# Optimization experiments

Measured on AMD Instinct MI355X. Metric: run time of the kernel, lower is better.

Reference implementation:

```python
import jax, jax.numpy as jnp
import numpy as np

B, T, E, H = 4, 2048, 1024, 16
D = E // H  # head_size = 64

def setup_inputs() -> dict:
    key = jax.random.key(0)
    ks = jax.random.split(key, 8)
    s = 1.0 / np.sqrt(E)
    inp = {
        'k': jax.random.normal(ks[0], (B, T, E), jnp.float32),
        'q': jax.random.normal(ks[1], (B, T, E), jnp.float32),
        'v': jax.random.normal(ks[2], (B, T, E), jnp.float32),
        'mask': jnp.triu(jnp.ones((T, T), jnp.bool_), k=1),  # True above diagonal -> masked
        # per-head projection weights stacked: [H, E, D], no bias (bias=False)
        'Wk': jax.random.uniform(ks[3], (H, E, D), jnp.float32, -s, s),
        'Wq': jax.random.uniform(ks[4], (H, E, D), jnp.float32, -s, s),
        'Wv': jax.random.uniform(ks[5], (H, E, D), jnp.float32, -s, s),
        # output projection (bias=True default)
        'Wp': jax.random.uniform(ks[6], (E, E), jnp.float32, -s, s),
        'bp': jax.random.uniform(ks[7], (E,), jnp.float32, -s, s),
    }
    return inp

def reference(k, q, v, mask, Wk, Wq, Wv, Wp, bp):
    # per-head projections (bias=False Linears), batched over heads
    xk = jnp.einsum('bte,hed->bhtd', k, Wk)
    xq = jnp.einsum('bte,hed->bhtd', q, Wq)
    xv = jnp.einsum('bte,hed->bhtd', v, Wv)
    # NOTE: original scales by sqrt(C) where C = embed_size (input dim), not head_size
    wei = jnp.einsum('bhtd,bhsd->bhts', xq, xk) / jnp.sqrt(jnp.asarray(E, xq.dtype))
    wei = jnp.where(mask, -jnp.inf, wei)  # masked_fill(mask, -inf)
    wei = jax.nn.softmax(wei, axis=-1)
    out = jnp.einsum('bhts,bhsd->bhtd', wei, xv)
    out = out.transpose(0, 2, 1, 3).reshape(B, T, E)  # concat heads on last dim
    return out @ Wp.T + bp
```

## Files before the change

kernel.cpp:

```cpp
#include <hip/hip_runtime.h>
#include <cstdint>
#include <cstddef>


#define B_ 4
#define T_ 2048
#define E_ 1024
#define H_ 16
#define D_ 64
#define MROWS 8192
#define MK    8388608
#define SCALE_LOG2E 0.045084220027780106f

typedef unsigned short u16;
typedef unsigned int   u32;
typedef __attribute__((ext_vector_type(4))) float  f32x4;
typedef __attribute__((ext_vector_type(4))) u32    u32x4;
typedef __attribute__((ext_vector_type(8))) u16    u16x8;
typedef __attribute__((ext_vector_type(8))) __bf16 bf16x8;

typedef __attribute__((address_space(1))) void gvoid_t;
typedef __attribute__((address_space(3))) void lvoid_t;

__device__ __forceinline__ void async_load16(const void* g, void* l) {
  __builtin_amdgcn_global_load_lds((gvoid_t*)(uintptr_t)g, (lvoid_t*)l, 16, 0, 0);
}

__device__ __forceinline__ u16 f2bf(float f) {
  u32 u = __builtin_bit_cast(u32, f);
  u = (u + 0x7FFFu + ((u >> 16) & 1u)) >> 16;
  return (u16)u;
}

__device__ __forceinline__ u16 f2bf_hw(float f) {
  return __builtin_bit_cast(u16, (__bf16)f);
}

__device__ __forceinline__ float fast_exp2(float x) {
#if __has_builtin(__builtin_amdgcn_exp2f)
  return __builtin_amdgcn_exp2f(x);
#else
  return exp2f(x);
#endif
}

__device__ __forceinline__ bf16x8 ldfrag(const u16* p) {
  u32x4 t = *(const u32x4*)p;
  return __builtin_bit_cast(bf16x8, t);
}

__device__ __forceinline__ bf16x8 ldfrag_g(const u16* p) {
  u32x4 t = *(const u32x4*)p;
  return __builtin_bit_cast(bf16x8, t);
}

__device__ __forceinline__ f32x4 mfma_bf16(bf16x8 a, bf16x8 b, f32x4 c) {
  return __builtin_amdgcn_mfma_f32_16x16x32_bf16(a, b, c, 0, 0, 0);
}

__global__ __launch_bounds__(256) void cast_qkv_kernel(
    const float* __restrict__ q, const float* __restrict__ k,
    const float* __restrict__ v, u16* __restrict__ dst) {
  const int z = blockIdx.y;
  const float* src = (z == 0) ? q : (z == 1) ? k : v;
  const float sc = (z == 0) ? SCALE_LOG2E : 1.0f;
  u16* out = dst + (size_t)z * MK;
  size_t i0 = ((size_t)blockIdx.x * 256 + threadIdx.x) * 8;
  float4 a = *(const float4*)(src + i0);
  float4 b = *(const float4*)(src + i0 + 4);
  u16x8 o;
  o[0] = f2bf_hw(a.x * sc); o[1] = f2bf_hw(a.y * sc);
  o[2] = f2bf_hw(a.z * sc); o[3] = f2bf_hw(a.w * sc);
  o[4] = f2bf_hw(b.x * sc); o[5] = f2bf_hw(b.y * sc);
  o[6] = f2bf_hw(b.z * sc); o[7] = f2bf_hw(b.w * sc);
  *(u16x8*)(out + i0) = o;
}

__global__ __launch_bounds__(256) void prep_weights_kernel(
    const float* __restrict__ Wq, const float* __restrict__ Wk,
    const float* __restrict__ Wv, const float* __restrict__ Wp,
    u16* __restrict__ dstW, u16* __restrict__ dstWp) {
  const int z = blockIdx.y;
  const int t = blockIdx.x * 256 + threadIdx.x;
  if (z == 3) { dstWp[t] = f2bf(Wp[t]); return; }
  const float* W = (z == 0) ? Wq : (z == 1) ? Wk : Wv;
  const int j = t >> 10, e = t & 1023;
  const int h = j >> 6, d = j & 63;
  dstW[(size_t)z * (E_ * E_) + t] = f2bf(W[h * (E_ * D_) + e * D_ + d]);
}

template <int FINAL>
__global__ __launch_bounds__(256) void gemm_bt_kernel(
    const u16* __restrict__ Abase, const u16* __restrict__ Btbase,
    u16* __restrict__ Cb, float* __restrict__ Cf,
    const float* __restrict__ bias) {
  constexpr int Md = 8192, Nd = 1024, Kd = 1024;
  __shared__ __align__(16) u16 As[128 * 32];
  __shared__ __align__(16) u16 Bs[128 * 32];
  const int tid = threadIdx.x;
  const int wave = tid >> 6, lane = tid & 63;
  const int l16 = lane & 15, quad = lane >> 4;
  const int z = blockIdx.z;
  const u16* A  = Abase  + (size_t)z * Md * Kd;
  const u16* Bt = Btbase + (size_t)z * Nd * Kd;
  const int tm = blockIdx.x * 128, tn = blockIdx.y * 128;
  const int wm = (wave >> 1) * 64, wn = (wave & 1) * 64;

  f32x4 acc[4][4];
#pragma unroll
  for (int i = 0; i < 4; ++i)
#pragma unroll
    for (int j = 0; j < 4; ++j) acc[i][j] = f32x4{0.f, 0.f, 0.f, 0.f};

  const int row0 = tid >> 2, seg = tid & 3;
  const u16* Ag0 = A  + (size_t)(tm + row0) * Kd + seg * 8;
  const u16* Ag1 = Ag0 + (size_t)64 * Kd;
  const u16* Bg0 = Bt + (size_t)(tn + row0) * Kd + seg * 8;
  const u16* Bg1 = Bg0 + (size_t)64 * Kd;
  char* AsB = (char*)&As[0];
  char* BsB = (char*)&Bs[0];
  const int wbase = wave * 1024;

  for (int kt = 0; kt < Kd / 32; ++kt) {
    async_load16(Ag0, AsB + wbase);
    async_load16(Ag1, AsB + 4096 + wbase);
    async_load16(Bg0, BsB + wbase);
    async_load16(Bg1, BsB + 4096 + wbase);
    Ag0 += 32; Ag1 += 32; Bg0 += 32; Bg1 += 32;
    __syncthreads();
    bf16x8 af[4], bfr[4];
#pragma unroll
    for (int i = 0; i < 4; ++i) {
      af[i]  = ldfrag(&As[(wm + i * 16 + l16) * 32 + quad * 8]);
      bfr[i] = ldfrag(&Bs[(wn + i * 16 + l16) * 32 + quad * 8]);
    }
#pragma unroll
    for (int mi = 0; mi < 4; ++mi)
#pragma unroll
      for (int ni = 0; ni < 4; ++ni)
        acc[mi][ni] = mfma_bf16(af[mi], bfr[ni], acc[mi][ni]);
    __syncthreads();
  }

  if (FINAL) {
    float bv[4];
#pragma unroll
    for (int ni = 0; ni < 4; ++ni) bv[ni] = bias[tn + wn + ni * 16 + l16];
#pragma unroll
    for (int mi = 0; mi < 4; ++mi)
#pragma unroll
      for (int r = 0; r < 4; ++r) {
        const int row = tm + wm + mi * 16 + quad * 4 + r;
        float* cp = Cf + (size_t)row * Nd + tn + wn;
#pragma unroll
        for (int ni = 0; ni < 4; ++ni)
          cp[ni * 16 + l16] = acc[mi][ni][r] + bv[ni];
      }
  } else {
    u16* C = Cb + (size_t)z * Md * Nd;
#pragma unroll
    for (int mi = 0; mi < 4; ++mi)
#pragma unroll
      for (int r = 0; r < 4; ++r) {
        const int row = tm + wm + mi * 16 + quad * 4 + r;
        u16* cp = C + (size_t)row * Nd + tn + wn;
#pragma unroll
        for (int ni = 0; ni < 4; ++ni)
          cp[ni * 16 + l16] = f2bf(acc[mi][ni][r]);
      }
  }
}

__global__ __launch_bounds__(256, 3) void attn_kernel(
    const u16* __restrict__ Xq, const u16* __restrict__ Xk,
    const u16* __restrict__ Xv, u16* __restrict__ Xo) {
  const int qt = 15 - blockIdx.y;
  const int bh = blockIdx.x;
  const int b = bh >> 4, h = bh & 15;
  const int tid = threadIdx.x, wave = tid >> 6, lane = tid & 63;
  const int l16 = lane & 15, quad = lane >> 4;

  __shared__ __align__(16) u16 Ks[2 * 4096];
  __shared__ __align__(16) u16 Vts[2 * 4608];
  __shared__ __align__(16) u16 Ps[128 * 72];

  const size_t base = (size_t)b * T_ * E_ + h * 64;
  const u16* Qp = Xq + base + (size_t)qt * 128 * E_;
  const u16* Kp = Xk + base;
  const u16* Vp = Xv + base;
  char* KsB = (char*)&Ks[0];

  const int kk8 = lane & 3;

  auto stageK = [&](int kt, int buf) {
#pragma unroll
    for (int i = 0; i < 2; ++i) {
      const int c = wave + i * 4;
      const int ks = c >> 2, rb = (c & 3) * 16;
      const int row = rb + (lane >> 2);
      async_load16(Kp + (size_t)(kt * 64 + row) * E_ + ks * 32 + kk8 * 8,
                   KsB + buf * 8192 + ks * 4096 + rb * 64);
    }
  };
  auto loadV = [&](int kt, u32x4* vreg) {
#pragma unroll
    for (int i = 0; i < 2; ++i) {
      const int dseg = wave + i * 4;
      vreg[i] = *(const u32x4*)(Vp + (size_t)(kt * 64 + lane) * E_ + dseg * 8);
    }
  };
  auto writeV = [&](int buf, const u32x4* vreg) {
#pragma unroll
    for (int i = 0; i < 2; ++i) {
      const int dseg = wave + i * 4;
      union { u32x4 v; u16 s[8]; } t; t.v = vreg[i];
#pragma unroll
      for (int ii = 0; ii < 8; ++ii)
        Vts[buf * 4608 + (dseg * 8 + ii) * 72 + lane] = t.s[ii];
    }
  };

  bf16x8 qf[2][2];
#pragma unroll
  for (int mi = 0; mi < 2; ++mi)
#pragma unroll
    for (int ks = 0; ks < 2; ++ks)
      qf[mi][ks] = ldfrag_g(Qp + (size_t)(wave * 32 + mi * 16 + l16) * E_ +
                            ks * 32 + quad * 8);

  u16x8 ones_u;
#pragma unroll
  for (int i = 0; i < 8; ++i) ones_u[i] = 0x3F80;
  const bf16x8 ones = __builtin_bit_cast(bf16x8, ones_u);

  f32x4 o_acc[2][4];
#pragma unroll
  for (int mi = 0; mi < 2; ++mi)
#pragma unroll
    for (int di = 0; di < 4; ++di) o_acc[mi][di] = f32x4{0.f, 0.f, 0.f, 0.f};
  f32x4 lrow[2] = {f32x4{0.f, 0.f, 0.f, 0.f}, f32x4{0.f, 0.f, 0.f, 0.f}};

  {
    u32x4 vreg[2];
    stageK(0, 0);
    loadV(0, vreg);
    writeV(0, vreg);
  }

  const int kt_end = 2 * qt + 1;
  for (int kt = 0; kt <= kt_end; ++kt) {
    const int buf = kt & 1;
    __syncthreads();

    bf16x8 kf[4][2];
#pragma unroll
    for (int ni = 0; ni < 4; ++ni)
#pragma unroll
      for (int ks = 0; ks < 2; ++ks)
        kf[ni][ks] = ldfrag(&Ks[buf * 4096 + ks * 2048 + (ni * 16 + l16) * 32 +
                                quad * 8]);

    f32x4 sa[2][4];
#pragma unroll
    for (int mi = 0; mi < 2; ++mi)
#pragma unroll
      for (int ni = 0; ni < 4; ++ni) {
        f32x4 s = f32x4{0.f, 0.f, 0.f, 0.f};
        s = mfma_bf16(qf[mi][0], kf[ni][0], s);
        s = mfma_bf16(qf[mi][1], kf[ni][1], s);
        sa[mi][ni] = s;
      }

    u32x4 vreg[2];
    const bool have_next = (kt < kt_end);
    if (have_next) {
      stageK(kt + 1, buf ^ 1);
      loadV(kt + 1, vreg);
    }

    if (kt >= 2 * qt) {
#pragma unroll
      for (int mi = 0; mi < 2; ++mi) {
        const int grow0 = qt * 128 + wave * 32 + mi * 16 + quad * 4;
#pragma unroll
        for (int ni = 0; ni < 4; ++ni) {
          const int gcol = kt * 64 + ni * 16 + l16;
#pragma unroll
          for (int r = 0; r < 4; ++r)
            if (gcol > grow0 + r) sa[mi][ni][r] = -INFINITY;
        }
      }
    }

#pragma unroll
    for (int mi = 0; mi < 2; ++mi) {
#pragma unroll
      for (int ni = 0; ni < 4; ++ni)
#pragma unroll
        for (int r = 0; r < 4; ++r)
          sa[mi][ni][r] = fast_exp2(sa[mi][ni][r]);
#pragma unroll
      for (int ni = 0; ni < 4; ++ni)
#pragma unroll
        for (int r = 0; r < 4; ++r)
          Ps[(wave * 32 + mi * 16 + quad * 4 + r) * 72 + ni * 16 + l16] =
              f2bf_hw(sa[mi][ni][r]);
    }

    if (have_next) writeV(buf ^ 1, vreg);

    bf16x8 pf[2][2], vf[4][2];
#pragma unroll
    for (int mi = 0; mi < 2; ++mi)
#pragma unroll
      for (int ks = 0; ks < 2; ++ks)
        pf[mi][ks] = ldfrag(&Ps[(wave * 32 + mi * 16 + l16) * 72 + ks * 32 +
                                quad * 8]);
#pragma unroll
    for (int di = 0; di < 4; ++di)
#pragma unroll
      for (int ks = 0; ks < 2; ++ks)
        vf[di][ks] = ldfrag(&Vts[buf * 4608 + (di * 16 + l16) * 72 + ks * 32 +
                                 quad * 8]);
#pragma unroll
    for (int mi = 0; mi < 2; ++mi) {
      lrow[mi] = mfma_bf16(pf[mi][0], ones, lrow[mi]);
      lrow[mi] = mfma_bf16(pf[mi][1], ones, lrow[mi]);
#pragma unroll
      for (int di = 0; di < 4; ++di) {
        o_acc[mi][di] = mfma_bf16(pf[mi][0], vf[di][0], o_acc[mi][di]);
        o_acc[mi][di] = mfma_bf16(pf[mi][1], vf[di][1], o_acc[mi][di]);
      }
    }
  }

  u16* Op = Xo + base + (size_t)qt * 128 * E_;
#pragma unroll
  for (int mi = 0; mi < 2; ++mi)
#pragma unroll
    for (int r = 0; r < 4; ++r) {
      const float inv = 1.0f / lrow[mi][r];
      const int row = wave * 32 + mi * 16 + quad * 4 + r;
#pragma unroll
      for (int di = 0; di < 4; ++di)
        Op[(size_t)row * E_ + di * 16 + l16] = f2bf_hw(o_acc[mi][di][r] * inv);
    }
}

extern "C" void kernel_launch(void* const* d_in, const int* in_sizes, int n_in,
                              void* d_out, int out_size, void* d_ws, size_t ws_size,
                              hipStream_t stream) {
  const float* k_in = (const float*)d_in[0];
  const float* q_in = (const float*)d_in[1];
  const float* v_in = (const float*)d_in[2];
  const float* Wk = (const float*)d_in[4];
  const float* Wq = (const float*)d_in[5];
  const float* Wv = (const float*)d_in[6];
  const float* Wp = (const float*)d_in[7];
  const float* bp = (const float*)d_in[8];
  float* out = (float*)d_out;

  char* ws = (char*)d_ws;
  u16* qkvb = (u16*)ws;
  u16* Wt   = (u16*)(ws + 50331648);
  u16* Wpb  = (u16*)(ws + 56623104);
  u16* X    = (u16*)(ws + 58720256);
  u16* Xo   = (u16*)ws;

  cast_qkv_kernel<<<dim3(4096, 3), 256, 0, stream>>>(q_in, k_in, v_in, qkvb);
  prep_weights_kernel<<<dim3(4096, 4), 256, 0, stream>>>(Wq, Wk, Wv, Wp, Wt, Wpb);
  gemm_bt_kernel<0><<<dim3(64, 8, 3), 256, 0, stream>>>(qkvb, Wt, X, nullptr, nullptr);
  attn_kernel<<<dim3(64, 16), 256, 0, stream>>>(X, X + (size_t)MK, X + (size_t)2 * MK, Xo);
  gemm_bt_kernel<1><<<dim3(64, 8, 1), 256, 0, stream>>>(Xo, Wpb, nullptr, out, bp);
}
```

Measured before the change: 326.9 us.

## Replace GEMM with 256x256 double-buffered pipelined kernel using swizzled LDS

Replaces the 128x128, single-buffered, K=32 GEMM with a 256x256-tile, 512-thread kernel. It stages K=64 slices into double-buffered LDS with an XOR swizzle and interleaves async global loads with the MFMA phases. Explicit vmcnt waits, sched barriers and setprio control the overlap. This targets barrier stalls, global-load latency and LDS bank conflicts in the projection GEMMs. The cost is more registers and LDS per block, and fewer blocks in flight.

```diff
diff --git a/kernel.cpp b/kernel.cpp
--- a/kernel.cpp
+++ b/kernel.cpp
@@ -90,64 +90,164 @@
 }
 
 template <int FINAL>
-__global__ __launch_bounds__(256) void gemm_bt_kernel(
+__global__ __launch_bounds__(512, 2) void gemm256_kernel(
     const u16* __restrict__ Abase, const u16* __restrict__ Btbase,
     u16* __restrict__ Cb, float* __restrict__ Cf,
     const float* __restrict__ bias) {
   constexpr int Md = 8192, Nd = 1024, Kd = 1024;
-  __shared__ __align__(16) u16 As[128 * 32];
-  __shared__ __align__(16) u16 Bs[128 * 32];
+  constexpr int NT = Kd / 64;
+  constexpr int NJ = NT / 2;
+  __shared__ __align__(16) u16 AS[2][16384];
+  __shared__ __align__(16) u16 BS[2][16384];
   const int tid = threadIdx.x;
   const int wave = tid >> 6, lane = tid & 63;
   const int l16 = lane & 15, quad = lane >> 4;
+  const int wm = (wave >> 2) * 128;
+  const int wn = (wave & 3) * 64;
   const int z = blockIdx.z;
   const u16* A  = Abase  + (size_t)z * Md * Kd;
   const u16* Bt = Btbase + (size_t)z * Nd * Kd;
-  const int tm = blockIdx.x * 128, tn = blockIdx.y * 128;
-  const int wm = (wave >> 1) * 64, wn = (wave & 1) * 64;
-
-  f32x4 acc[4][4];
-#pragma unroll
-  for (int i = 0; i < 4; ++i)
-#pragma unroll
-    for (int j = 0; j < 4; ++j) acc[i][j] = f32x4{0.f, 0.f, 0.f, 0.f};
-
-  const int row0 = tid >> 2, seg = tid & 3;
-  const u16* Ag0 = A  + (size_t)(tm + row0) * Kd + seg * 8;
-  const u16* Ag1 = Ag0 + (size_t)64 * Kd;
-  const u16* Bg0 = Bt + (size_t)(tn + row0) * Kd + seg * 8;
-  const u16* Bg1 = Bg0 + (size_t)64 * Kd;
-  char* AsB = (char*)&As[0];
-  char* BsB = (char*)&Bs[0];
-  const int wbase = wave * 1024;
-
-  for (int kt = 0; kt < Kd / 32; ++kt) {
-    async_load16(Ag0, AsB + wbase);
-    async_load16(Ag1, AsB + 4096 + wbase);
-    async_load16(Bg0, BsB + wbase);
-    async_load16(Bg1, BsB + 4096 + wbase);
-    Ag0 += 32; Ag1 += 32; Bg0 += 32; Bg1 += 32;
-    __syncthreads();
-    bf16x8 af[4], bfr[4];
-#pragma unroll
-    for (int i = 0; i < 4; ++i) {
-      af[i]  = ldfrag(&As[(wm + i * 16 + l16) * 32 + quad * 8]);
-      bfr[i] = ldfrag(&Bs[(wn + i * 16 + l16) * 32 + quad * 8]);
-    }
+  const int tm = blockIdx.x * 256, tn = blockIdx.y * 256;
+
+  f32x4 acc[8][4];
+#pragma unroll
+  for (int i = 0; i < 8; ++i)
+#pragma unroll
+    for (int jj = 0; jj < 4; ++jj) acc[i][jj] = f32x4{0.f, 0.f, 0.f, 0.f};
+
+  char* ASB = (char*)&AS[0][0];
+  char* BSB = (char*)&BS[0][0];
+  const int r8  = lane >> 3;
+  const int csw = (lane & 7) ^ r8;
+  const int srow = wave * 8 + r8;
+
+  auto stA = [&](int t, int q) {
+    if (t < NT)
+      async_load16(A + (size_t)(tm + q * 64 + srow) * Kd + t * 64 + csw * 8,
+                   ASB + (t & 1) * 32768 + q * 8192 + wave * 1024);
+  };
+  auto stB = [&](int t, int q) {
+    if (t < NT)
+      async_load16(Bt + (size_t)(tn + q * 64 + srow) * Kd + t * 64 + csw * 8,
+                   BSB + (t & 1) * 32768 + q * 8192 + wave * 1024);
+  };
+  auto ldA = [&](int buf, int mi, int ks) -> bf16x8 {
+    const int row = wm + mi * 16 + l16;
+    const int ch  = (ks * 4 + quad) ^ (l16 & 7);
+    return ldfrag(&AS[buf][row * 64 + ch * 8]);
+  };
+  auto ldB = [&](int buf, int ni, int ks) -> bf16x8 {
+    const int row = wn + ni * 16 + l16;
+    const int ch  = (ks * 4 + quad) ^ (l16 & 7);
+    return ldfrag(&BS[buf][row * 64 + ch * 8]);
+  };
+
+  bf16x8 af[4][2], bf[4][2];
+
+#define GBAR() __builtin_amdgcn_s_barrier()
+#define PHASE_END()                       \
+  __builtin_amdgcn_sched_barrier(0);      \
+  GBAR()
+#define MFMA_QUAD(MB, NB)                                                   \
+  __builtin_amdgcn_s_setprio(1);                                            \
+  _Pragma("unroll") for (int mi = 0; mi < 4; ++mi)                          \
+  _Pragma("unroll") for (int ni = 0; ni < 2; ++ni)                          \
+  _Pragma("unroll") for (int ks = 0; ks < 2; ++ks)                          \
+      acc[(MB) + mi][(NB) + ni] = mfma_bf16(                                \
+          af[mi][ks], bf[(NB) + ni][ks], acc[(MB) + mi][(NB) + ni]);        \
+  __builtin_amdgcn_s_setprio(0)
+
+  stA(0, 0); stA(0, 2); stB(0, 0); stB(0, 1);
+  stA(0, 1); stA(0, 3); stB(0, 2); stB(0, 3);
+  stA(1, 0); stA(1, 2); stB(1, 0); stB(1, 1); stA(1, 1); stA(1, 3);
+  asm volatile("s_waitcnt vmcnt(6)" ::: "memory");
+  GBAR();
+
+  for (int j = 0; j < NJ; ++j) {
+    const int u = 2 * j;
 #pragma unroll
     for (int mi = 0; mi < 4; ++mi)
 #pragma unroll
-      for (int ni = 0; ni < 4; ++ni)
-        acc[mi][ni] = mfma_bf16(af[mi], bfr[ni], acc[mi][ni]);
-    __syncthreads();
+      for (int ks = 0; ks < 2; ++ks) af[mi][ks] = ldA(0, mi, ks);
+#pragma unroll
+    for (int ni = 0; ni < 2; ++ni)
+#pragma unroll
+      for (int ks = 0; ks < 2; ++ks) bf[ni][ks] = ldB(0, ni, ks);
+    stB(u + 1, 2); stB(u + 1, 3);
+    GBAR();
+    MFMA_QUAD(0, 0);
+    PHASE_END();
+#pragma unroll
+    for (int ni = 2; ni < 4; ++ni)
+#pragma unroll
+      for (int ks = 0; ks < 2; ++ks) bf[ni][ks] = ldB(0, ni, ks);
+    stA(u + 2, 0); stA(u + 2, 2);
+    GBAR();
+    MFMA_QUAD(0, 2);
+    PHASE_END();
+#pragma unroll
+    for (int mi = 0; mi < 4; ++mi)
+#pragma unroll
+      for (int ks = 0; ks < 2; ++ks) af[mi][ks] = ldA(0, mi + 4, ks);
+    stB(u + 2, 0); stB(u + 2, 1);
+    GBAR();
+    MFMA_QUAD(4, 0);
+    PHASE_END();
+    stA(u + 2, 1); stA(u + 2, 3);
+    GBAR();
+    MFMA_QUAD(4, 2);
+    __builtin_amdgcn_sched_barrier(0);
+    if (j == NJ - 1) {
+      asm volatile("s_waitcnt vmcnt(0)" ::: "memory");
+    } else {
+      asm volatile("s_waitcnt vmcnt(6)" ::: "memory");
+    }
+    GBAR();
+#pragma unroll
+    for (int mi = 0; mi < 4; ++mi)
+#pragma unroll
+      for (int ks = 0; ks < 2; ++ks) af[mi][ks] = ldA(1, mi, ks);
+#pragma unroll
+    for (int ni = 0; ni < 2; ++ni)
+#pragma unroll
+      for (int ks = 0; ks < 2; ++ks) bf[ni][ks] = ldB(1, ni, ks);
+    stB(u + 2, 2); stB(u + 2, 3);
+    GBAR();
+    MFMA_QUAD(0, 0);
+    PHASE_END();
+#pragma unroll
+    for (int ni = 2; ni < 4; ++ni)
+#pragma unroll
+      for (int ks = 0; ks < 2; ++ks) bf[ni][ks] = ldB(1, ni, ks);
+    stA(u + 3, 0); stA(u + 3, 2);
+    GBAR();
+    MFMA_QUAD(0, 2);
+    PHASE_END();
+#pragma unroll
+    for (int mi = 0; mi < 4; ++mi)
+#pragma unroll
+      for (int ks = 0; ks < 2; ++ks) af[mi][ks] = ldA(1, mi + 4, ks);
+    stB(u + 3, 0); stB(u + 3, 1);
+    GBAR();
+    MFMA_QUAD(4, 0);
+    PHASE_END();
+    stA(u + 3, 1); stA(u + 3, 3);
+    GBAR();
+    MFMA_QUAD(4, 2);
+    __builtin_amdgcn_sched_barrier(0);
+    asm volatile("s_waitcnt vmcnt(6)" ::: "memory");
+    GBAR();
   }
+#undef MFMA_QUAD
+#undef PHASE_END
+#undef GBAR
 
   if (FINAL) {
     float bv[4];
 #pragma unroll
     for (int ni = 0; ni < 4; ++ni) bv[ni] = bias[tn + wn + ni * 16 + l16];
 #pragma unroll
-    for (int mi = 0; mi < 4; ++mi)
+    for (int mi = 0; mi < 8; ++mi)
 #pragma unroll
       for (int r = 0; r < 4; ++r) {
         const int row = tm + wm + mi * 16 + quad * 4 + r;
@@ -159,7 +259,7 @@
   } else {
     u16* C = Cb + (size_t)z * Md * Nd;
 #pragma unroll
-    for (int mi = 0; mi < 4; ++mi)
+    for (int mi = 0; mi < 8; ++mi)
 #pragma unroll
       for (int r = 0; r < 4; ++r) {
         const int row = tm + wm + mi * 16 + quad * 4 + r;
@@ -369,7 +469,7 @@
 
   cast_qkv_kernel<<<dim3(4096, 3), 256, 0, stream>>>(q_in, k_in, v_in, qkvb);
   prep_weights_kernel<<<dim3(4096, 4), 256, 0, stream>>>(Wq, Wk, Wv, Wp, Wt, Wpb);
-  gemm_bt_kernel<0><<<dim3(64, 8, 3), 256, 0, stream>>>(qkvb, Wt, X, nullptr, nullptr);
+  gemm256_kernel<0><<<dim3(32, 4, 3), 512, 0, stream>>>(qkvb, Wt, X, nullptr, nullptr);
   attn_kernel<<<dim3(64, 16), 256, 0, stream>>>(X, X + (size_t)MK, X + (size_t)2 * MK, Xo);
-  gemm_bt_kernel<1><<<dim3(64, 8, 1), 256, 0, stream>>>(Xo, Wpb, nullptr, out, bp);
-}
+  gemm256_kernel<1><<<dim3(32, 4, 1), 512, 0, stream>>>(Xo, Wpb, nullptr, out, bp);
+}
```

After: 337.7 us. 1.03x slower.

## Double GEMM K-tile to 64 with XOR-swizzled LDS, add MFMA priority hints

Applied to the files above, without the earlier changes.

The bf16 GEMM now stages a 64-wide K slice per iteration instead of 32, which halves the number of barrier pairs and loop iterations. Global-to-LDS loads are laid out with an XOR swizzle on 16-byte chunks, and the fragment reads apply the same swizzle to avoid LDS bank conflicts on the wider 128-byte rows. The GEMM epilogue switches to the hardware bf16 conversion. In the attention kernel, s_setprio raises wave priority around the MFMA blocks so other waves' memory work can interleave. The cost is doubled LDS per GEMM block, which may lower occupancy.

```diff
diff --git a/kernel.cpp b/kernel.cpp
--- a/kernel.cpp
+++ b/kernel.cpp
@@ -95,8 +95,8 @@
     u16* __restrict__ Cb, float* __restrict__ Cf,
     const float* __restrict__ bias) {
   constexpr int Md = 8192, Nd = 1024, Kd = 1024;
-  __shared__ __align__(16) u16 As[128 * 32];
-  __shared__ __align__(16) u16 Bs[128 * 32];
+  __shared__ __align__(16) u16 As[128 * 64];
+  __shared__ __align__(16) u16 Bs[128 * 64];
   const int tid = threadIdx.x;
   const int wave = tid >> 6, lane = tid & 63;
   const int l16 = lane & 15, quad = lane >> 4;
@@ -112,33 +112,40 @@
 #pragma unroll
     for (int j = 0; j < 4; ++j) acc[i][j] = f32x4{0.f, 0.f, 0.f, 0.f};
 
-  const int row0 = tid >> 2, seg = tid & 3;
-  const u16* Ag0 = A  + (size_t)(tm + row0) * Kd + seg * 8;
-  const u16* Ag1 = Ag0 + (size_t)64 * Kd;
-  const u16* Bg0 = Bt + (size_t)(tn + row0) * Kd + seg * 8;
-  const u16* Bg1 = Bg0 + (size_t)64 * Kd;
+  const int r8  = lane >> 3;
+  const int csw = (lane & 7) ^ r8;
+  const u16* Ag = A  + (size_t)(tm + wave * 8 + r8) * Kd + csw * 8;
+  const u16* Bg = Bt + (size_t)(tn + wave * 8 + r8) * Kd + csw * 8;
   char* AsB = (char*)&As[0];
   char* BsB = (char*)&Bs[0];
-  const int wbase = wave * 1024;
-
-  for (int kt = 0; kt < Kd / 32; ++kt) {
-    async_load16(Ag0, AsB + wbase);
-    async_load16(Ag1, AsB + 4096 + wbase);
-    async_load16(Bg0, BsB + wbase);
-    async_load16(Bg1, BsB + 4096 + wbase);
-    Ag0 += 32; Ag1 += 32; Bg0 += 32; Bg1 += 32;
+  const int dst0 = wave * 1024;
+
+  const int xr = l16 & 7;
+
+  for (int kt = 0; kt < Kd / 64; ++kt) {
+#pragma unroll
+    for (int i = 0; i < 4; ++i)
+      async_load16(Ag + (size_t)i * 32 * Kd, AsB + i * 4096 + dst0);
+#pragma unroll
+    for (int i = 0; i < 4; ++i)
+      async_load16(Bg + (size_t)i * 32 * Kd, BsB + i * 4096 + dst0);
+    Ag += 64; Bg += 64;
     __syncthreads();
-    bf16x8 af[4], bfr[4];
-#pragma unroll
-    for (int i = 0; i < 4; ++i) {
-      af[i]  = ldfrag(&As[(wm + i * 16 + l16) * 32 + quad * 8]);
-      bfr[i] = ldfrag(&Bs[(wn + i * 16 + l16) * 32 + quad * 8]);
-    }
-#pragma unroll
-    for (int mi = 0; mi < 4; ++mi)
-#pragma unroll
-      for (int ni = 0; ni < 4; ++ni)
-        acc[mi][ni] = mfma_bf16(af[mi], bfr[ni], acc[mi][ni]);
+#pragma unroll
+    for (int ks = 0; ks < 2; ++ks) {
+      bf16x8 af[4], bfr[4];
+#pragma unroll
+      for (int i = 0; i < 4; ++i) {
+        const int ch = (ks * 4 + quad) ^ xr;
+        af[i]  = ldfrag(&As[(wm + i * 16 + l16) * 64 + ch * 8]);
+        bfr[i] = ldfrag(&Bs[(wn + i * 16 + l16) * 64 + ch * 8]);
+      }
+#pragma unroll
+      for (int mi = 0; mi < 4; ++mi)
+#pragma unroll
+        for (int ni = 0; ni < 4; ++ni)
+          acc[mi][ni] = mfma_bf16(af[mi], bfr[ni], acc[mi][ni]);
+    }
     __syncthreads();
   }
 
@@ -166,7 +173,7 @@
         u16* cp = C + (size_t)row * Nd + tn + wn;
 #pragma unroll
         for (int ni = 0; ni < 4; ++ni)
-          cp[ni * 16 + l16] = f2bf(acc[mi][ni][r]);
+          cp[ni * 16 + l16] = f2bf_hw(acc[mi][ni][r]);
       }
   }
 }
@@ -261,6 +268,7 @@
                                 quad * 8]);
 
     f32x4 sa[2][4];
+    __builtin_amdgcn_s_setprio(1);
 #pragma unroll
     for (int mi = 0; mi < 2; ++mi)
 #pragma unroll
@@ -270,6 +278,7 @@
         s = mfma_bf16(qf[mi][1], kf[ni][1], s);
         sa[mi][ni] = s;
       }
+    __builtin_amdgcn_s_setprio(0);
 
     u32x4 vreg[2];
     const bool have_next = (kt < kt_end);
@@ -322,6 +331,7 @@
       for (int ks = 0; ks < 2; ++ks)
         vf[di][ks] = ldfrag(&Vts[buf * 4608 + (di * 16 + l16) * 72 + ks * 32 +
                                  quad * 8]);
+    __builtin_amdgcn_s_setprio(1);
 #pragma unroll
     for (int mi = 0; mi < 2; ++mi) {
       lrow[mi] = mfma_bf16(pf[mi][0], ones, lrow[mi]);
@@ -332,6 +342,7 @@
         o_acc[mi][di] = mfma_bf16(pf[mi][1], vf[di][1], o_acc[mi][di]);
       }
     }
+    __builtin_amdgcn_s_setprio(0);
   }
 
   u16* Op = Xo + base + (size_t)qt * 128 * E_;
```

New measurement: 315.2 us. -3.6%, faster.
